# Optimization experiments

Hardware: AMD Instinct MI355X
Metric: run time of the kernel (lower is better)

The kernel has to match this reference:

```python
import jax, jax.numpy as jnp
import numpy as np

N_NODES = 100000
N_EDGES = 1600000
D = 128


def sage_conv(x, src, dst, W_l, W_r, b):
    # mean aggregation of source-node features at destination nodes
    msgs = x[src]  # [E, D] gather
    agg = jax.ops.segment_sum(msgs, dst, num_segments=N_NODES)  # [N, D]
    deg = jax.ops.segment_sum(jnp.ones((src.shape[0],), x.dtype), dst,
                              num_segments=N_NODES)
    agg = agg / jnp.maximum(deg, 1.0)[:, None]
    # PyG SAGEConv: lin_l(agg) + lin_r(x) (bias lives in lin_l)
    return agg @ W_l + x @ W_r + b


def setup_inputs() -> dict:
    key = jax.random.key(0)
    ks = jax.random.split(key, 8)
    s = 1.0 / np.sqrt(D)
    x = jax.random.normal(ks[0], (N_NODES, D), dtype=jnp.float32)
    edge_index = jax.random.randint(ks[1], (2, N_EDGES), 0, N_NODES, dtype=jnp.int64)
    W_l1 = jax.random.normal(ks[2], (D, D), dtype=jnp.float32) * s
    W_r1 = jax.random.normal(ks[3], (D, D), dtype=jnp.float32) * s
    b1 = jnp.zeros((D,), dtype=jnp.float32)
    W_l2 = jax.random.normal(ks[4], (D, D), dtype=jnp.float32) * s
    W_r2 = jax.random.normal(ks[5], (D, D), dtype=jnp.float32) * s
    b2 = jnp.zeros((D,), dtype=jnp.float32)
    return {"x": x, "edge_index": edge_index, "W_l1": W_l1, "W_r1": W_r1,
            "b1": b1, "W_l2": W_l2, "W_r2": W_r2, "b2": b2}


def reference(x, edge_index, W_l1, W_r1, b1, W_l2, W_r2, b2):
    src, dst = edge_index[0], edge_index[1]
    h = jax.nn.relu(sage_conv(x, src, dst, W_l1, W_r1, b1))
    h = jax.nn.relu(sage_conv(h, src, dst, W_l2, W_r2, b2))
    return h
```

## Files before the change

### kernel.cpp

```cpp
#include <hip/hip_runtime.h>
#include <hip/hip_bf16.h>
#include <stdint.h>

#define D 128
#define BCAP 18432
#define CPAD 32
typedef unsigned short u16;
typedef unsigned int u32;
typedef __attribute__((ext_vector_type(8))) short bf16x8;
typedef __attribute__((ext_vector_type(4))) float f32x4;
typedef __attribute__((ext_vector_type(2))) float f32x2;
typedef __attribute__((ext_vector_type(2))) unsigned int u32x2;

__device__ inline u16 f_to_bf16(float f) {
    u32 u = __builtin_bit_cast(u32, f);
    u += 0x7FFFu + ((u >> 16) & 1u);
    return (u16)(u >> 16);
}
__device__ inline u32 pack_bf16(float a, float b) {
    return (u32)f_to_bf16(a) | ((u32)f_to_bf16(b) << 16);
}

__global__ void zero_ints(int* __restrict__ p, int n) {
    int i = blockIdx.x * blockDim.x + threadIdx.x;
    if (i < n) p[i] = 0;
}

__global__ __launch_bounds__(256) void prep_fused(
    const int* __restrict__ src, const int* __restrict__ dst, int E, int nbuck, int binB,
    uint2* __restrict__ pairs, int* __restrict__ bcur,
    const float* __restrict__ x, u16* __restrict__ xb, int nf4, int convB,
    const float* __restrict__ Wl1, const float* __restrict__ Wr1,
    const float* __restrict__ Wl2, const float* __restrict__ Wr2,
    u16* __restrict__ WT1, u16* __restrict__ WT2) {
    __shared__ int hist[128], gb[128], loc[128];
    int tid = threadIdx.x;
    int bid = blockIdx.x;
    if (bid < binB) {
        if (tid < 128) { hist[tid] = 0; loc[tid] = 0; }
        __syncthreads();
        int base = bid * 4096;
        int d[16], b[16];
        #pragma unroll
        for (int i = 0; i < 16; ++i) {
            int e = base + i * 256 + tid;
            d[i] = (e < E) ? dst[e] : -1;
            b[i] = (d[i] >= 0) ? (d[i] >> 10) : -1;
            if (b[i] >= 0) atomicAdd(&hist[b[i]], 1);
        }
        __syncthreads();
        if (tid < nbuck && hist[tid] > 0) gb[tid] = atomicAdd(&bcur[tid * CPAD], hist[tid]);
        __syncthreads();
        #pragma unroll
        for (int i = 0; i < 16; ++i) {
            if (b[i] >= 0) {
                int e = base + i * 256 + tid;
                int s = src[e];
                int r = atomicAdd(&loc[b[i]], 1);
                int pos = gb[b[i]] + r;
                if (pos < BCAP)
                    pairs[(size_t)b[i] * BCAP + pos] = make_uint2((u32)s, (u32)d[i]);
            }
        }
    } else if (bid < binB + convB) {
        int idx = (bid - binB) * 256 + tid;
        int stride = convB * 256;
        const float4* xf = (const float4*)x;
        uint2* xo = (uint2*)xb;
        for (int i = idx; i < nf4; i += stride) {
            float4 v = xf[i];
            xo[i] = make_uint2(pack_bf16(v.x, v.y), pack_bf16(v.z, v.w));
        }
    } else {
        int id = (bid - binB - convB) * 256 + tid;
        if (id < 2 * 128 * 256) {
            int which = id >> 15;
            int rem = id & 32767;
            int n = rem >> 8;
            int k = rem & 255;
            const float* Wl = which ? Wl2 : Wl1;
            const float* Wr = which ? Wr2 : Wr1;
            float v = (k < 128) ? Wl[k * 128 + n] : Wr[(k - 128) * 128 + n];
            u16* WT = which ? WT2 : WT1;
            WT[n * 256 + k] = f_to_bf16(v);
        }
    }
}

__global__ __launch_bounds__(1024) void build_csr(
    const uint2* __restrict__ pairs, const int* __restrict__ bcur, int N,
    int* __restrict__ cnt, int* __restrict__ seg_start, int* __restrict__ gtotal,
    int* __restrict__ csr_src) {
    __shared__ int cnt_l[1024];
    __shared__ int off_l[1024];
    __shared__ int sblk[1024];
    __shared__ int gbase_s;
    int tid = threadIdx.x;
    int bk = blockIdx.x;
    int n0 = bk << 10;
    int nN = min(1024, N - n0);
    cnt_l[tid] = 0;
    __syncthreads();
    int m = min(bcur[bk * CPAD], BCAP);
    const uint2* P = pairs + (size_t)bk * BCAP;
    for (int i = tid; i < m; i += 1024) {
        uint2 p = P[i];
        atomicAdd(&cnt_l[(int)p.y - n0], 1);
    }
    __syncthreads();
    int c = cnt_l[tid];
    sblk[tid] = c;
    for (int off = 1; off < 1024; off <<= 1) {
        __syncthreads();
        int u = (tid >= off) ? sblk[tid - off] : 0;
        __syncthreads();
        sblk[tid] += u;
    }
    int excl = sblk[tid] - c;
    off_l[tid] = excl;
    if (tid == 1023) gbase_s = atomicAdd(gtotal, sblk[1023]);
    __syncthreads();
    int gbase = gbase_s;
    if (tid < nN) {
        cnt[n0 + tid] = c;
        seg_start[n0 + tid] = gbase + excl;
    }
    cnt_l[tid] = 0;
    __syncthreads();
    for (int i = tid; i < m; i += 1024) {
        uint2 p = P[i];
        int dl = (int)p.y - n0;
        int r = atomicAdd(&cnt_l[dl], 1);
        csr_src[gbase + off_l[dl] + r] = (int)p.x;
    }
}

__global__ __launch_bounds__(256) void aggregate_bf16(
    const u16* __restrict__ xb, const int* __restrict__ csr_src,
    const int* __restrict__ seg_start, const int* __restrict__ cnt,
    int N, u16* __restrict__ agg) {
    int wave = threadIdx.x >> 6;
    int lane = threadIdx.x & 63;
    int n = blockIdx.x * (blockDim.x >> 6) + wave;
    if (n >= N) return;
    int s0 = seg_start[n];
    int deg = cnt[n];
    int sub = lane & 15;
    int eoff = lane >> 4;

    f32x2 acc2[4];
    #pragma unroll
    for (int i = 0; i < 4; ++i) acc2[i] = (f32x2){0.f, 0.f};

    for (int c0 = 0; c0 < deg; c0 += 64) {
        int chunkN = min(deg - c0, 64);
        int myidx = (lane < chunkN) ? csr_src[s0 + c0 + lane] : 0;
        for (int e0 = 0; e0 < chunkN; e0 += 16) {
            uint4 v[4];
            #pragma unroll
            for (int j = 0; j < 4; ++j) {
                int ej = e0 + j * 4 + eoff;
                if (e0 + j * 4 < chunkN) {
                    int s = __shfl(myidx, ej & 63);
                    if (ej < chunkN)
                        v[j] = ((const uint4*)(xb + (size_t)s * 128))[sub];
                }
            }
            #pragma unroll
            for (int j = 0; j < 4; ++j) {
                int ej = e0 + j * 4 + eoff;
                if (ej < chunkN) {
                    u32 w;
                    w = v[j].x; acc2[0] += __builtin_bit_cast(f32x2, (u32x2){w << 16, w & 0xFFFF0000u});
                    w = v[j].y; acc2[1] += __builtin_bit_cast(f32x2, (u32x2){w << 16, w & 0xFFFF0000u});
                    w = v[j].z; acc2[2] += __builtin_bit_cast(f32x2, (u32x2){w << 16, w & 0xFFFF0000u});
                    w = v[j].w; acc2[3] += __builtin_bit_cast(f32x2, (u32x2){w << 16, w & 0xFFFF0000u});
                }
            }
        }
    }

    float a[8];
    #pragma unroll
    for (int i = 0; i < 4; ++i) { a[2 * i] = acc2[i].x; a[2 * i + 1] = acc2[i].y; }
    #pragma unroll
    for (int i = 0; i < 8; ++i) {
        a[i] += __shfl_xor(a[i], 16);
        a[i] += __shfl_xor(a[i], 32);
    }

    if (eoff == 0) {
        float inv = 1.0f / fmaxf((float)deg, 1.0f);
        uint4 o;
        o.x = pack_bf16(a[0] * inv, a[1] * inv);
        o.y = pack_bf16(a[2] * inv, a[3] * inv);
        o.z = pack_bf16(a[4] * inv, a[5] * inv);
        o.w = pack_bf16(a[6] * inv, a[7] * inv);
        ((uint4*)(agg + (size_t)n * 128))[sub] = o;
    }
}

template<int OUT_BF16>
__global__ __launch_bounds__(256) void sage_gemm(
    const u16* __restrict__ Aa, const u16* __restrict__ Ax,
    const u16* __restrict__ WT, const float* __restrict__ bias,
    void* __restrict__ out, int N) {
    __shared__ u16 Bl[128 * 256];
    int tid = threadIdx.x;

    {
        const uint4* Wg = (const uint4*)WT;
        uint4* Bl4 = (uint4*)Bl;
        #pragma unroll
        for (int i = 0; i < 16; ++i) {
            int cid = tid + 256 * i;
            int n = cid >> 5;
            int kc = cid & 31;
            Bl4[(n << 5) | (kc ^ (n & 15))] = Wg[cid];
        }
    }
    __syncthreads();

    int wavein = tid >> 6;
    int lane = tid & 63;
    int col = lane & 15;
    int chunk = lane >> 4;
    int wid = blockIdx.x * 4 + wavein;

    size_t m0 = (size_t)wid * 32 + col;
    size_t m1 = m0 + 16;
    size_t m0c = (m0 < (size_t)N) ? m0 : (size_t)(N - 1);
    size_t m1c = (m1 < (size_t)N) ? m1 : (size_t)(N - 1);

    const bf16x8* a0p = (const bf16x8*)(Aa + m0c * 128 + chunk * 8);
    const bf16x8* a1p = (const bf16x8*)(Aa + m1c * 128 + chunk * 8);
    const bf16x8* x0p = (const bf16x8*)(Ax + m0c * 128 + chunk * 8);
    const bf16x8* x1p = (const bf16x8*)(Ax + m1c * 128 + chunk * 8);

    f32x4 acc0[8], acc1[8];
    #pragma unroll
    for (int t = 0; t < 8; ++t) {
        acc0[t] = (f32x4){0.f, 0.f, 0.f, 0.f};
        acc1[t] = (f32x4){0.f, 0.f, 0.f, 0.f};
    }

    #pragma unroll
    for (int s = 0; s < 4; ++s) {
        bf16x8 a0 = a0p[s * 4];
        bf16x8 a1 = a1p[s * 4];
        int kc = s * 4 + chunk;
        #pragma unroll
        for (int t = 0; t < 8; ++t) {
            const bf16x8* bp = (const bf16x8*)(Bl + (((16 * t + col) << 8) | ((kc ^ col) << 3)));
            bf16x8 b = *bp;
            acc0[t] = __builtin_amdgcn_mfma_f32_16x16x32_bf16(a0, b, acc0[t], 0, 0, 0);
            acc1[t] = __builtin_amdgcn_mfma_f32_16x16x32_bf16(a1, b, acc1[t], 0, 0, 0);
        }
    }
    #pragma unroll
    for (int s = 0; s < 4; ++s) {
        bf16x8 a0 = x0p[s * 4];
        bf16x8 a1 = x1p[s * 4];
        int kc = 16 + s * 4 + chunk;
        #pragma unroll
        for (int t = 0; t < 8; ++t) {
            const bf16x8* bp = (const bf16x8*)(Bl + (((16 * t + col) << 8) | ((kc ^ col) << 3)));
            bf16x8 b = *bp;
            acc0[t] = __builtin_amdgcn_mfma_f32_16x16x32_bf16(a0, b, acc0[t], 0, 0, 0);
            acc1[t] = __builtin_amdgcn_mfma_f32_16x16x32_bf16(a1, b, acc1[t], 0, 0, 0);
        }
    }

    #pragma unroll
    for (int mt = 0; mt < 2; ++mt) {
        size_t row0 = (size_t)wid * 32 + mt * 16 + chunk * 4;
        #pragma unroll
        for (int t = 0; t < 8; ++t) {
            int n = 16 * t + col;
            float bv = bias[n];
            f32x4 a = mt ? acc1[t] : acc0[t];
            #pragma unroll
            for (int r = 0; r < 4; ++r) {
                size_t row = row0 + r;
                if (row < (size_t)N) {
                    float v = fmaxf(a[r] + bv, 0.f);
                    if (OUT_BF16) ((u16*)out)[row * 128 + n] = f_to_bf16(v);
                    else          ((float*)out)[row * 128 + n] = v;
                }
            }
        }
    }
}

extern "C" void kernel_launch(void* const* d_in, const int* in_sizes, int n_in,
                              void* d_out, int out_size, void* d_ws, size_t ws_size,
                              hipStream_t stream) {
    const float* x   = (const float*)d_in[0];
    const int*   ei  = (const int*)d_in[1];
    const float* Wl1 = (const float*)d_in[2];
    const float* Wr1 = (const float*)d_in[3];
    const float* b1  = (const float*)d_in[4];
    const float* Wl2 = (const float*)d_in[5];
    const float* Wr2 = (const float*)d_in[6];
    const float* b2  = (const float*)d_in[7];
    float* out       = (float*)d_out;

    int N = in_sizes[0] / D;
    int E = in_sizes[1] / 2;
    const int* src = ei;
    const int* dst = ei + E;
    int nbuck = (N + 1023) >> 10;

    char* ws = (char*)d_ws;
    int* cnt       = (int*)ws;  ws += (size_t)N * 4;
    int* seg_start = (int*)ws;  ws += (size_t)N * 4;
    int* bcur      = (int*)ws;  ws += 128 * CPAD * 4;
    int* gtotal    = (int*)ws;  ws += 4 * 4;
    ws = (char*)(((uintptr_t)ws + 255) & ~(uintptr_t)255);
    int* csr_src   = (int*)ws;  ws += (size_t)E * 4;
    ws = (char*)(((uintptr_t)ws + 255) & ~(uintptr_t)255);
    u16* WT1       = (u16*)ws;  ws += (size_t)128 * 256 * 2;
    u16* WT2       = (u16*)ws;  ws += (size_t)128 * 256 * 2;
    ws = (char*)(((uintptr_t)ws + 255) & ~(uintptr_t)255);
    u16* aggb      = (u16*)ws;  ws += (size_t)N * 128 * 2;
    ws = (char*)(((uintptr_t)ws + 255) & ~(uintptr_t)255);
    u16* h1b       = (u16*)ws;  ws += (size_t)N * 128 * 2;
    u16* xb        = (u16*)d_out;
    uint2* pairs   = (uint2*)aggb;

    zero_ints<<<(128 * CPAD + 4 + 255) / 256, 256, 0, stream>>>(bcur, 128 * CPAD + 4);

    int binB  = (E + 4095) / 4096;
    int convB = 2048;
    int nf4   = N * (D / 4);
    prep_fused<<<binB + convB + 256, 256, 0, stream>>>(
        src, dst, E, nbuck, binB, pairs, bcur,
        x, xb, nf4, convB, Wl1, Wr1, Wl2, Wr2, WT1, WT2);

    build_csr<<<nbuck, 1024, 0, stream>>>(pairs, bcur, N, cnt, seg_start, gtotal, csr_src);

    int aggBlocks = (N + 3) / 4;
    int gemmBlocks = (N + 127) / 128;

    aggregate_bf16<<<aggBlocks, 256, 0, stream>>>(xb, csr_src, seg_start, cnt, N, aggb);
    sage_gemm<1><<<gemmBlocks, 256, 0, stream>>>(aggb, xb, WT1, b1, h1b, N);

    aggregate_bf16<<<aggBlocks, 256, 0, stream>>>(h1b, csr_src, seg_start, cnt, N, aggb);
    sage_gemm<0><<<gemmBlocks, 256, 0, stream>>>(aggb, h1b, WT2, b2, out, N);
}
```

Baseline: 327.5 us.

## Pack edge pairs into 32 bits, stage CSR scatter and GEMM epilogue in LDS

Edge pairs are packed as src<<10 | local dst in one 32-bit word, halving the bucket traffic. build_csr now places the source ids into a shared-memory staging buffer, in two halves, before writing the CSR array with coalesced stores. The GEMM epilogue writes its results through swizzled LDS so that each thread emits contiguous 16-byte row stores instead of scattered scalar stores. This adds LDS use and extra barriers, and relies on src fitting in 22 bits and each half-bucket holding at most HCAP edges.

```diff
diff --git a/kernel.cpp b/kernel.cpp
--- a/kernel.cpp
+++ b/kernel.cpp
@@ -5,6 +5,7 @@
 #define D 128
 #define BCAP 18432
 #define CPAD 32
+#define HCAP 9216
 typedef unsigned short u16;
 typedef unsigned int u32;
 typedef __attribute__((ext_vector_type(8))) short bf16x8;
@@ -28,7 +29,7 @@
 
 __global__ __launch_bounds__(256) void prep_fused(
     const int* __restrict__ src, const int* __restrict__ dst, int E, int nbuck, int binB,
-    uint2* __restrict__ pairs, int* __restrict__ bcur,
+    u32* __restrict__ pairs, int* __restrict__ bcur,
     const float* __restrict__ x, u16* __restrict__ xb, int nf4, int convB,
     const float* __restrict__ Wl1, const float* __restrict__ Wr1,
     const float* __restrict__ Wl2, const float* __restrict__ Wr2,
@@ -59,7 +60,7 @@
                 int r = atomicAdd(&loc[b[i]], 1);
                 int pos = gb[b[i]] + r;
                 if (pos < BCAP)
-                    pairs[(size_t)b[i] * BCAP + pos] = make_uint2((u32)s, (u32)d[i]);
+                    pairs[(size_t)b[i] * BCAP + pos] = ((u32)s << 10) | ((u32)d[i] & 1023u);
             }
         }
     } else if (bid < binB + convB) {
@@ -88,12 +89,13 @@
 }
 
 __global__ __launch_bounds__(1024) void build_csr(
-    const uint2* __restrict__ pairs, const int* __restrict__ bcur, int N,
+    const u32* __restrict__ pairs, const int* __restrict__ bcur, int N,
     int* __restrict__ cnt, int* __restrict__ seg_start, int* __restrict__ gtotal,
     int* __restrict__ csr_src) {
     __shared__ int cnt_l[1024];
     __shared__ int off_l[1024];
     __shared__ int sblk[1024];
+    __shared__ u32 stage[HCAP];
     __shared__ int gbase_s;
     int tid = threadIdx.x;
     int bk = blockIdx.x;
@@ -102,10 +104,9 @@
     cnt_l[tid] = 0;
     __syncthreads();
     int m = min(bcur[bk * CPAD], BCAP);
-    const uint2* P = pairs + (size_t)bk * BCAP;
+    const u32* P = pairs + (size_t)bk * BCAP;
     for (int i = tid; i < m; i += 1024) {
-        uint2 p = P[i];
-        atomicAdd(&cnt_l[(int)p.y - n0], 1);
+        atomicAdd(&cnt_l[P[i] & 1023u], 1);
     }
     __syncthreads();
     int c = cnt_l[tid];
@@ -125,13 +126,29 @@
         cnt[n0 + tid] = c;
         seg_start[n0 + tid] = gbase + excl;
     }
-    cnt_l[tid] = 0;
-    __syncthreads();
-    for (int i = tid; i < m; i += 1024) {
-        uint2 p = P[i];
-        int dl = (int)p.y - n0;
-        int r = atomicAdd(&cnt_l[dl], 1);
-        csr_src[gbase + off_l[dl] + r] = (int)p.x;
+    int total = sblk[1023];
+    int hstart1 = off_l[512];
+    __syncthreads();
+    #pragma unroll
+    for (int half = 0; half < 2; ++half) {
+        int hstart = half ? hstart1 : 0;
+        int hcount = half ? (total - hstart1) : hstart1;
+        if (hcount > HCAP) hcount = HCAP;
+        if (tid < 512) cnt_l[tid] = 0;
+        __syncthreads();
+        for (int i = tid; i < m; i += 1024) {
+            u32 e = P[i];
+            int dl = (int)(e & 1023u);
+            if ((dl >> 9) == half) {
+                int r = atomicAdd(&cnt_l[dl & 511], 1);
+                int idx = off_l[dl] - hstart + r;
+                if (idx < HCAP) stage[idx] = e >> 10;
+            }
+        }
+        __syncthreads();
+        for (int j = tid; j < hcount; j += 1024)
+            csr_src[gbase + hstart + j] = (int)stage[j];
+        __syncthreads();
     }
 }
 
@@ -271,21 +288,52 @@
         }
     }
 
-    #pragma unroll
-    for (int mt = 0; mt < 2; ++mt) {
-        size_t row0 = (size_t)wid * 32 + mt * 16 + chunk * 4;
-        #pragma unroll
-        for (int t = 0; t < 8; ++t) {
-            int n = 16 * t + col;
-            float bv = bias[n];
-            f32x4 a = mt ? acc1[t] : acc0[t];
+    __syncthreads();
+    float* stg = (float*)Bl;
+    {
+        int bRowBase = wavein * 32;
+        #pragma unroll
+        for (int mt = 0; mt < 2; ++mt) {
             #pragma unroll
-            for (int r = 0; r < 4; ++r) {
-                size_t row = row0 + r;
-                if (row < (size_t)N) {
-                    float v = fmaxf(a[r] + bv, 0.f);
-                    if (OUT_BF16) ((u16*)out)[row * 128 + n] = f_to_bf16(v);
-                    else          ((float*)out)[row * 128 + n] = v;
+            for (int t = 0; t < 8; ++t) {
+                int n = 16 * t + col;
+                float bv = bias[n];
+                f32x4 a = mt ? acc1[t] : acc0[t];
+                #pragma unroll
+                for (int r = 0; r < 4; ++r) {
+                    int br = bRowBase + mt * 16 + chunk * 4 + r;
+                    stg[br * 128 + (n ^ ((br & 31) << 2))] = fmaxf(a[r] + bv, 0.f);
+                }
+            }
+        }
+    }
+    __syncthreads();
+    {
+        int row = tid >> 1;
+        int half = tid & 1;
+        size_t grow = (size_t)blockIdx.x * 128 + row;
+        if (grow < (size_t)N) {
+            int sw = (row & 31) << 2;
+            if (OUT_BF16) {
+                uint4* op = (uint4*)((u16*)out + grow * 128 + half * 64);
+                #pragma unroll
+                for (int qq = 0; qq < 16; qq += 2) {
+                    f32x4 v0 = *(const f32x4*)&stg[row * 128 + ((half * 64 + qq * 4) ^ sw)];
+                    f32x4 v1 = *(const f32x4*)&stg[row * 128 + ((half * 64 + qq * 4 + 4) ^ sw)];
+                    uint4 o;
+                    o.x = pack_bf16(v0[0], v0[1]);
+                    o.y = pack_bf16(v0[2], v0[3]);
+                    o.z = pack_bf16(v1[0], v1[1]);
+                    o.w = pack_bf16(v1[2], v1[3]);
+                    op[qq >> 1] = o;
+                }
+            } else {
+                float4* op = (float4*)((float*)out + grow * 128 + half * 64);
+                #pragma unroll
+                for (int q = 0; q < 16; ++q) {
+                    f32x4 v = *(const f32x4*)&stg[row * 128 + ((half * 64 + q * 4) ^ sw)];
+                    float4 o = make_float4(v[0], v[1], v[2], v[3]);
+                    op[q] = o;
                 }
             }
         }
@@ -326,7 +374,7 @@
     ws = (char*)(((uintptr_t)ws + 255) & ~(uintptr_t)255);
     u16* h1b       = (u16*)ws;  ws += (size_t)N * 128 * 2;
     u16* xb        = (u16*)d_out;
-    uint2* pairs   = (uint2*)aggb;
+    u32* pairs     = (u32*)aggb;
 
     zero_ints<<<(128 * CPAD + 4 + 255) / 256, 256, 0, stream>>>(bcur, 128 * CPAD + 4);
 
```

After: 355.2 us. 1.08x slower.

## Slice aggregation by feature columns, pack edge pairs, stage CSR scatter in LDS

Applied to the files above, without the earlier changes.

The aggregation kernel now splits the 128 features into 8 slices of 16 columns. Each block handles one slice for a contiguous chunk of nodes, so a block's gathers touch only a 2 MB column slice of the feature table, which should improve L2/cache locality. Edge pairs are packed into a single 32-bit word (source shifted by 10, destination low bits), halving pair traffic. The CSR scatter is staged in shared memory in two halves so writes to csr_src are coalesced. Risks: each gather is now a 4-byte load per lane instead of 16 bytes, giving many more small memory requests. Packing assumes source ids below 2^22, and the HCAP clipping can drop edges if a half-bucket is overloaded.

```diff
diff --git a/kernel.cpp b/kernel.cpp
--- a/kernel.cpp
+++ b/kernel.cpp
@@ -5,6 +5,7 @@
 #define D 128
 #define BCAP 18432
 #define CPAD 32
+#define HCAP 9216
 typedef unsigned short u16;
 typedef unsigned int u32;
 typedef __attribute__((ext_vector_type(8))) short bf16x8;
@@ -28,7 +29,7 @@
 
 __global__ __launch_bounds__(256) void prep_fused(
     const int* __restrict__ src, const int* __restrict__ dst, int E, int nbuck, int binB,
-    uint2* __restrict__ pairs, int* __restrict__ bcur,
+    u32* __restrict__ pairs, int* __restrict__ bcur,
     const float* __restrict__ x, u16* __restrict__ xb, int nf4, int convB,
     const float* __restrict__ Wl1, const float* __restrict__ Wr1,
     const float* __restrict__ Wl2, const float* __restrict__ Wr2,
@@ -59,7 +60,7 @@
                 int r = atomicAdd(&loc[b[i]], 1);
                 int pos = gb[b[i]] + r;
                 if (pos < BCAP)
-                    pairs[(size_t)b[i] * BCAP + pos] = make_uint2((u32)s, (u32)d[i]);
+                    pairs[(size_t)b[i] * BCAP + pos] = ((u32)s << 10) | ((u32)d[i] & 1023u);
             }
         }
     } else if (bid < binB + convB) {
@@ -88,12 +89,13 @@
 }
 
 __global__ __launch_bounds__(1024) void build_csr(
-    const uint2* __restrict__ pairs, const int* __restrict__ bcur, int N,
+    const u32* __restrict__ pairs, const int* __restrict__ bcur, int N,
     int* __restrict__ cnt, int* __restrict__ seg_start, int* __restrict__ gtotal,
     int* __restrict__ csr_src) {
     __shared__ int cnt_l[1024];
     __shared__ int off_l[1024];
     __shared__ int sblk[1024];
+    __shared__ u32 stage[HCAP];
     __shared__ int gbase_s;
     int tid = threadIdx.x;
     int bk = blockIdx.x;
@@ -102,10 +104,9 @@
     cnt_l[tid] = 0;
     __syncthreads();
     int m = min(bcur[bk * CPAD], BCAP);
-    const uint2* P = pairs + (size_t)bk * BCAP;
+    const u32* P = pairs + (size_t)bk * BCAP;
     for (int i = tid; i < m; i += 1024) {
-        uint2 p = P[i];
-        atomicAdd(&cnt_l[(int)p.y - n0], 1);
+        atomicAdd(&cnt_l[P[i] & 1023u], 1);
     }
     __syncthreads();
     int c = cnt_l[tid];
@@ -125,78 +126,69 @@
         cnt[n0 + tid] = c;
         seg_start[n0 + tid] = gbase + excl;
     }
-    cnt_l[tid] = 0;
-    __syncthreads();
-    for (int i = tid; i < m; i += 1024) {
-        uint2 p = P[i];
-        int dl = (int)p.y - n0;
-        int r = atomicAdd(&cnt_l[dl], 1);
-        csr_src[gbase + off_l[dl] + r] = (int)p.x;
-    }
-}
-
-__global__ __launch_bounds__(256) void aggregate_bf16(
+    int total = sblk[1023];
+    int hstart1 = off_l[512];
+    __syncthreads();
+    #pragma unroll
+    for (int half = 0; half < 2; ++half) {
+        int hstart = half ? hstart1 : 0;
+        int hcount = half ? (total - hstart1) : hstart1;
+        if (hcount > HCAP) hcount = HCAP;
+        if (tid < 512) cnt_l[tid] = 0;
+        __syncthreads();
+        for (int i = tid; i < m; i += 1024) {
+            u32 e = P[i];
+            int dl = (int)(e & 1023u);
+            if ((dl >> 9) == half) {
+                int r = atomicAdd(&cnt_l[dl & 511], 1);
+                int idx = off_l[dl] - hstart + r;
+                if (idx < HCAP) stage[idx] = e >> 10;
+            }
+        }
+        __syncthreads();
+        for (int j = tid; j < hcount; j += 1024)
+            csr_src[gbase + hstart + j] = (int)stage[j];
+        __syncthreads();
+    }
+}
+
+__global__ __launch_bounds__(256) void aggregate_sliced(
     const u16* __restrict__ xb, const int* __restrict__ csr_src,
     const int* __restrict__ seg_start, const int* __restrict__ cnt,
-    int N, u16* __restrict__ agg) {
+    int N, int chunks, u16* __restrict__ agg) {
+    int slice = blockIdx.x & 7;
+    int chunk = blockIdx.x >> 3;
     int wave = threadIdx.x >> 6;
     int lane = threadIdx.x & 63;
-    int n = blockIdx.x * (blockDim.x >> 6) + wave;
-    if (n >= N) return;
-    int s0 = seg_start[n];
-    int deg = cnt[n];
-    int sub = lane & 15;
-    int eoff = lane >> 4;
-
-    f32x2 acc2[4];
-    #pragma unroll
-    for (int i = 0; i < 4; ++i) acc2[i] = (f32x2){0.f, 0.f};
-
-    for (int c0 = 0; c0 < deg; c0 += 64) {
-        int chunkN = min(deg - c0, 64);
-        int myidx = (lane < chunkN) ? csr_src[s0 + c0 + lane] : 0;
-        for (int e0 = 0; e0 < chunkN; e0 += 16) {
-            uint4 v[4];
-            #pragma unroll
-            for (int j = 0; j < 4; ++j) {
-                int ej = e0 + j * 4 + eoff;
-                if (e0 + j * 4 < chunkN) {
-                    int s = __shfl(myidx, ej & 63);
-                    if (ej < chunkN)
-                        v[j] = ((const uint4*)(xb + (size_t)s * 128))[sub];
+    int sub = lane & 7;
+    int eoff = lane >> 3;
+    int npc = (N + chunks - 1) / chunks;
+    int nbeg = chunk * npc;
+    int nend = min(nbeg + npc, N);
+
+    for (int n = nbeg + wave; n < nend; n += 4) {
+        int s0 = seg_start[n];
+        int deg = cnt[n];
+        f32x2 acc = (f32x2){0.f, 0.f};
+        for (int c0 = 0; c0 < deg; c0 += 64) {
+            int chunkN = min(deg - c0, 64);
+            int myidx = (lane < chunkN) ? csr_src[s0 + c0 + lane] : 0;
+            for (int e0 = 0; e0 < chunkN; e0 += 8) {
+                int ej = e0 + eoff;
+                int s = __shfl(myidx, ej & 63);
+                if (ej < chunkN) {
+                    u32 w = *(const u32*)(xb + (size_t)s * 128 + slice * 16 + sub * 2);
+                    acc += __builtin_bit_cast(f32x2, (u32x2){w << 16, w & 0xFFFF0000u});
                 }
             }
-            #pragma unroll
-            for (int j = 0; j < 4; ++j) {
-                int ej = e0 + j * 4 + eoff;
-                if (ej < chunkN) {
-                    u32 w;
-                    w = v[j].x; acc2[0] += __builtin_bit_cast(f32x2, (u32x2){w << 16, w & 0xFFFF0000u});
-                    w = v[j].y; acc2[1] += __builtin_bit_cast(f32x2, (u32x2){w << 16, w & 0xFFFF0000u});
-                    w = v[j].z; acc2[2] += __builtin_bit_cast(f32x2, (u32x2){w << 16, w & 0xFFFF0000u});
-                    w = v[j].w; acc2[3] += __builtin_bit_cast(f32x2, (u32x2){w << 16, w & 0xFFFF0000u});
-                }
-            }
-        }
-    }
-
-    float a[8];
-    #pragma unroll
-    for (int i = 0; i < 4; ++i) { a[2 * i] = acc2[i].x; a[2 * i + 1] = acc2[i].y; }
-    #pragma unroll
-    for (int i = 0; i < 8; ++i) {
-        a[i] += __shfl_xor(a[i], 16);
-        a[i] += __shfl_xor(a[i], 32);
-    }
-
-    if (eoff == 0) {
-        float inv = 1.0f / fmaxf((float)deg, 1.0f);
-        uint4 o;
-        o.x = pack_bf16(a[0] * inv, a[1] * inv);
-        o.y = pack_bf16(a[2] * inv, a[3] * inv);
-        o.z = pack_bf16(a[4] * inv, a[5] * inv);
-        o.w = pack_bf16(a[6] * inv, a[7] * inv);
-        ((uint4*)(agg + (size_t)n * 128))[sub] = o;
+        }
+        acc.x += __shfl_xor(acc.x, 8);  acc.y += __shfl_xor(acc.y, 8);
+        acc.x += __shfl_xor(acc.x, 16); acc.y += __shfl_xor(acc.y, 16);
+        acc.x += __shfl_xor(acc.x, 32); acc.y += __shfl_xor(acc.y, 32);
+        if (eoff == 0) {
+            float inv = 1.0f / fmaxf((float)deg, 1.0f);
+            *(u32*)(agg + (size_t)n * 128 + slice * 16 + sub * 2) = pack_bf16(acc.x * inv, acc.y * inv);
+        }
     }
 }
 
@@ -326,7 +318,7 @@
     ws = (char*)(((uintptr_t)ws + 255) & ~(uintptr_t)255);
     u16* h1b       = (u16*)ws;  ws += (size_t)N * 128 * 2;
     u16* xb        = (u16*)d_out;
-    uint2* pairs   = (uint2*)aggb;
+    u32* pairs     = (u32*)aggb;
 
     zero_ints<<<(128 * CPAD + 4 + 255) / 256, 256, 0, stream>>>(bcur, 128 * CPAD + 4);
 
@@ -339,12 +331,12 @@
 
     build_csr<<<nbuck, 1024, 0, stream>>>(pairs, bcur, N, cnt, seg_start, gtotal, csr_src);
 
-    int aggBlocks = (N + 3) / 4;
+    int chunks = 256;
     int gemmBlocks = (N + 127) / 128;
 
-    aggregate_bf16<<<aggBlocks, 256, 0, stream>>>(xb, csr_src, seg_start, cnt, N, aggb);
+    aggregate_sliced<<<8 * chunks, 256, 0, stream>>>(xb, csr_src, seg_start, cnt, N, chunks, aggb);
     sage_gemm<1><<<gemmBlocks, 256, 0, stream>>>(aggb, xb, WT1, b1, h1b, N);
 
-    aggregate_bf16<<<aggBlocks, 256, 0, stream>>>(h1b, csr_src, seg_start, cnt, N, aggb);
+    aggregate_sliced<<<8 * chunks, 256, 0, stream>>>(h1b, csr_src, seg_start, cnt, N, chunks, aggb);
     sage_gemm<0><<<gemmBlocks, 256, 0, stream>>>(aggb, h1b, WT2, b2, out, N);
 }
```

New measurement: 644.1 us. +96.6%, slower.

## Pack edge pairs into 32 bits and stage CSR scatter in shared memory

Applied to the files above, without the earlier changes.

Each bucketed edge pair is packed into a single u32 holding the source index shifted left by 10 and the local destination in the low 10 bits, which halves the traffic for writing and re-reading pairs. In build_csr the scatter into csr_src now goes through a shared-memory staging buffer, processed in two halves of 512 destinations, so the global writes become contiguous coalesced stores instead of random ones. In exchange the pairs buffer is read three times instead of twice and the block gains a 36KB LDS footprint. The packing assumes source indices fit in 22 bits, and HCAP truncation silently drops edges if a half-bucket holds more than 9216 of them.

```diff
diff --git a/kernel.cpp b/kernel.cpp
--- a/kernel.cpp
+++ b/kernel.cpp
@@ -5,6 +5,7 @@
 #define D 128
 #define BCAP 18432
 #define CPAD 32
+#define HCAP 9216
 typedef unsigned short u16;
 typedef unsigned int u32;
 typedef __attribute__((ext_vector_type(8))) short bf16x8;
@@ -28,7 +29,7 @@
 
 __global__ __launch_bounds__(256) void prep_fused(
     const int* __restrict__ src, const int* __restrict__ dst, int E, int nbuck, int binB,
-    uint2* __restrict__ pairs, int* __restrict__ bcur,
+    u32* __restrict__ pairs, int* __restrict__ bcur,
     const float* __restrict__ x, u16* __restrict__ xb, int nf4, int convB,
     const float* __restrict__ Wl1, const float* __restrict__ Wr1,
     const float* __restrict__ Wl2, const float* __restrict__ Wr2,
@@ -59,7 +60,7 @@
                 int r = atomicAdd(&loc[b[i]], 1);
                 int pos = gb[b[i]] + r;
                 if (pos < BCAP)
-                    pairs[(size_t)b[i] * BCAP + pos] = make_uint2((u32)s, (u32)d[i]);
+                    pairs[(size_t)b[i] * BCAP + pos] = ((u32)s << 10) | ((u32)d[i] & 1023u);
             }
         }
     } else if (bid < binB + convB) {
@@ -88,12 +89,13 @@
 }
 
 __global__ __launch_bounds__(1024) void build_csr(
-    const uint2* __restrict__ pairs, const int* __restrict__ bcur, int N,
+    const u32* __restrict__ pairs, const int* __restrict__ bcur, int N,
     int* __restrict__ cnt, int* __restrict__ seg_start, int* __restrict__ gtotal,
     int* __restrict__ csr_src) {
     __shared__ int cnt_l[1024];
     __shared__ int off_l[1024];
     __shared__ int sblk[1024];
+    __shared__ u32 stage[HCAP];
     __shared__ int gbase_s;
     int tid = threadIdx.x;
     int bk = blockIdx.x;
@@ -102,10 +104,9 @@
     cnt_l[tid] = 0;
     __syncthreads();
     int m = min(bcur[bk * CPAD], BCAP);
-    const uint2* P = pairs + (size_t)bk * BCAP;
+    const u32* P = pairs + (size_t)bk * BCAP;
     for (int i = tid; i < m; i += 1024) {
-        uint2 p = P[i];
-        atomicAdd(&cnt_l[(int)p.y - n0], 1);
+        atomicAdd(&cnt_l[P[i] & 1023u], 1);
     }
     __syncthreads();
     int c = cnt_l[tid];
@@ -125,13 +126,29 @@
         cnt[n0 + tid] = c;
         seg_start[n0 + tid] = gbase + excl;
     }
-    cnt_l[tid] = 0;
-    __syncthreads();
-    for (int i = tid; i < m; i += 1024) {
-        uint2 p = P[i];
-        int dl = (int)p.y - n0;
-        int r = atomicAdd(&cnt_l[dl], 1);
-        csr_src[gbase + off_l[dl] + r] = (int)p.x;
+    int total = sblk[1023];
+    int hstart1 = off_l[512];
+    __syncthreads();
+    #pragma unroll
+    for (int half = 0; half < 2; ++half) {
+        int hstart = half ? hstart1 : 0;
+        int hcount = half ? (total - hstart1) : hstart1;
+        if (hcount > HCAP) hcount = HCAP;
+        if (tid < 512) cnt_l[tid] = 0;
+        __syncthreads();
+        for (int i = tid; i < m; i += 1024) {
+            u32 e = P[i];
+            int dl = (int)(e & 1023u);
+            if ((dl >> 9) == half) {
+                int r = atomicAdd(&cnt_l[dl & 511], 1);
+                int idx = off_l[dl] - hstart + r;
+                if (idx < HCAP) stage[idx] = e >> 10;
+            }
+        }
+        __syncthreads();
+        for (int j = tid; j < hcount; j += 1024)
+            csr_src[gbase + hstart + j] = (int)stage[j];
+        __syncthreads();
     }
 }
 
@@ -326,7 +343,7 @@
     ws = (char*)(((uintptr_t)ws + 255) & ~(uintptr_t)255);
     u16* h1b       = (u16*)ws;  ws += (size_t)N * 128 * 2;
     u16* xb        = (u16*)d_out;
-    uint2* pairs   = (uint2*)aggb;
+    u32* pairs     = (u32*)aggb;
 
     zero_ints<<<(128 * CPAD + 4 + 255) / 256, 256, 0, stream>>>(bcur, 128 * CPAD + 4);
 
```

Measured after the change: 322.2 us. Within noise of the previous version (-1.6%).
